# Performance work log

Measured on AMD Instinct MI355X. Metric: run time of the kernel, lower is better.

The kernel has to match this reference:

```python
import jax, jax.numpy as jnp
import numpy as np

N, D, R, E, B = 98304, 128, 3, 491520, 16384


def setup_inputs() -> dict:
    key = jax.random.key(0)
    ks = jax.random.split(key, 12)
    s = 0.05
    return {
        "latents": jax.random.normal(ks[0], (N, D), jnp.float32),
        "Wm": jax.random.normal(ks[1], (R, D, 2 * D), jnp.float32) * s,
        "bm": jax.random.normal(ks[2], (R, D), jnp.float32) * s,
        "W1": jax.random.normal(ks[3], (D, D), jnp.float32) * s,
        "b1": jax.random.normal(ks[4], (D,), jnp.float32) * s,
        "W2": jax.random.normal(ks[5], (D, D), jnp.float32) * s,
        "b2": jax.random.normal(ks[6], (D,), jnp.float32) * s,
        "message_from": jax.random.randint(ks[7], (E,), 0, N),
        "message_to": jax.random.randint(ks[8], (E,), 0, N),
        "view_id": jax.random.randint(ks[9], (N,), 0, B),
        "ch": 6,
        "batch_size": B,
    }


def reference(latents, Wm, bm, W1, b1, W2, b2, message_from, message_to, view_id, ch, batch_size):
    # Message passing rounds: gather -> concat -> Linear+ReLU (dropout=identity in eval) -> scale -> scatter-add
    scale = 1.0 / (ch - 1)
    for r in range(Wm.shape[0]):
        h = jnp.concatenate([latents[message_from], latents[message_to]], axis=-1)  # [E, 2D]
        msg = jax.nn.relu(h @ Wm[r].T + bm[r]) * scale  # [E, D]
        latents = latents.at[message_to].add(msg)
    # Readout: sum latents per sample (note: original's `/ ch` result is discarded, so no division)
    y = jax.ops.segment_sum(latents, view_id, num_segments=batch_size)  # [B, D]
    h = jax.nn.relu(y @ W1.T + b1)
    return h @ W2.T + b2
```

## Files before the change

kernel.cpp:

```cpp
#include <hip/hip_runtime.h>

static constexpr int N  = 98304;
static constexpr int D  = 128;
static constexpr int E  = 491520;
static constexpr int B  = 16384;

using f32x4 = __attribute__((ext_vector_type(4))) float;
using s16x8 = __attribute__((ext_vector_type(8))) short;

typedef __attribute__((address_space(3))) void lds_void;
typedef const __attribute__((address_space(1))) void gbl_void;

__device__ __forceinline__ ushort f2bf(float x) {
    unsigned u = __float_as_uint(x);
    return (ushort)((u + 0x7fffu + ((u >> 16) & 1u)) >> 16);
}
__device__ __forceinline__ float bflo(unsigned u) { return __uint_as_float(u << 16); }
__device__ __forceinline__ float bfhi(unsigned u) { return __uint_as_float(u & 0xffff0000u); }

__global__ void zero2_kernel(int* __restrict__ p) {
    int i = blockIdx.x * 256 + threadIdx.x;
    if (i < N + B) p[i] = 0;
}

__global__ void hist2_kernel(const int* __restrict__ eto, const int* __restrict__ view,
                             int* __restrict__ cnt, int* __restrict__ vcnt) {
    int gid = blockIdx.x * 256 + threadIdx.x;
    if (gid < E) atomicAdd(&cnt[eto[gid]], 1);
    else if (gid < E + N) atomicAdd(&vcnt[view[gid - E]], 1);
}

__global__ __launch_bounds__(256) void scan1_kernel(const int* __restrict__ cnt, int* __restrict__ excl,
                                                    const int* __restrict__ vcnt, int* __restrict__ vexcl,
                                                    int* __restrict__ bsum) {
    __shared__ int s[256];
    const int b = blockIdx.x, t = threadIdx.x;
    const int* src; int* dst; int base;
    bool pad = (b < 96);
    if (pad) { src = cnt;  dst = excl;  base = b * 1024 + t * 4; }
    else     { src = vcnt; dst = vexcl; base = (b - 96) * 1024 + t * 4; }
    int4 v = *reinterpret_cast<const int4*>(src + base);
    if (pad) { v.x = (v.x + 3) & ~3; v.y = (v.y + 3) & ~3; v.z = (v.z + 3) & ~3; v.w = (v.w + 3) & ~3; }
    int local = v.x + v.y + v.z + v.w;
    s[t] = local; __syncthreads();
    for (int off = 1; off < 256; off <<= 1) {
        int x = (t >= off) ? s[t - off] : 0;
        __syncthreads();
        s[t] += x;
        __syncthreads();
    }
    int excl_t = s[t] - local;
    if (t == 255) bsum[b] = s[t];
    int4 o;
    o.x = excl_t; o.y = o.x + v.x; o.z = o.y + v.y; o.w = o.z + v.z;
    *reinterpret_cast<int4*>(dst + base) = o;
}

__global__ __launch_bounds__(128) void scan2_kernel(int* __restrict__ bsum) {
    __shared__ int s[128];
    const int t = threadIdx.x;
    int val = (t < 112) ? bsum[t] : 0;
    s[t] = val;
    __syncthreads();
    #pragma unroll
    for (int off = 1; off < 128; off <<= 1) {
        int x = (t >= off) ? s[t - off] : 0;
        __syncthreads();
        s[t] += x;
        __syncthreads();
    }
    int incl = s[t];
    int seg0_total = s[95];
    int excl = incl - val;
    if (t < 96) bsum[t] = excl;
    else if (t < 112) bsum[t] = excl - seg0_total;
}

__global__ void scan3_kernel(int* __restrict__ excl, int* __restrict__ vexcl,
                             const int* __restrict__ bsum) {
    int b = blockIdx.x, t = threadIdx.x;
    if (b < 384) { int i = b * 256 + t; excl[i] += bsum[i >> 10]; }
    else         { int i = (b - 384) * 256 + t; vexcl[i] += bsum[96 + (i >> 10)]; }
}

__global__ void scatter2_kernel(const int* __restrict__ efrom, const int* __restrict__ eto,
                                const int* __restrict__ view,
                                int* __restrict__ ecur, int* __restrict__ vcur,
                                int* __restrict__ sfrom, int* __restrict__ perm) {
    int gid = blockIdx.x * 256 + threadIdx.x;
    if (gid < E) {
        int p = atomicAdd(&ecur[eto[gid]], 1);
        sfrom[p] = efrom[gid];
    } else if (gid < E + N) {
        int n = gid - E;
        int p = atomicAdd(&vcur[view[n]], 1);
        perm[p] = n;
    }
}

__global__ void fillpad_kernel(const int* __restrict__ cur, int* __restrict__ sfrom) {
    int v = blockIdx.x * 256 + threadIdx.x;
    if (v >= N) return;
    int c = cur[v], e = (c + 3) & ~3;
    for (; c < e; ++c) sfrom[c] = N;
}

__global__ void sentinel_kernel(ushort* __restrict__ Z) {
    Z[(size_t)N * 256 + threadIdx.x] = 0xFF80;
}

__global__ void convUV_kernel(const float* __restrict__ Wm, ushort* __restrict__ Wf) {
    int gid = blockIdx.x * 256 + threadIdx.x;
    if (gid >= 3 * 32768) return;
    int r = gid >> 15, rem = gid & 32767;
    int j = rem & 7, lane = (rem >> 3) & 63, grp = rem >> 9;
    int kt = grp >> 4, nt = grp & 15;
    int n = (nt & 7) * 16 + (lane & 15);
    int k = kt * 32 + (lane >> 4) * 8 + j;
    int col = ((nt >> 3) << 7) + k;
    Wf[gid] = f2bf(Wm[((size_t)r * 128 + n) * 256 + col]);
}

__global__ void convW12_kernel(const float* __restrict__ W1, const float* __restrict__ W2,
                               ushort* __restrict__ Wb12) {
    int gid = blockIdx.x * 256 + threadIdx.x;
    if (gid >= 2 * 16384) return;
    int w = gid >> 14, rem = gid & 16383;
    int n = rem >> 7, k = rem & 127;
    int kt = k >> 5, nt = n >> 4;
    int lane = (n & 15) + (((k >> 3) & 3) << 4);
    int j = k & 7;
    const float* W = w ? W2 : W1;
    Wb12[w * 16384 + ((kt * 8 + nt) * 64 + lane) * 8 + j] = f2bf(W[rem]);
}

__global__ __launch_bounds__(512) void uv_kernel(
    const float* __restrict__ Asrc, ushort* __restrict__ Z,
    const ushort* __restrict__ Wft, const float* __restrict__ bm_r)
{
    __shared__ alignas(16) ushort wlds[32768];
    const int t = threadIdx.x;

    #pragma unroll
    for (int it = 0; it < 8; ++it) {
        int idx = t + it * 512;
        __builtin_amdgcn_global_load_lds((gbl_void*)(Wft + idx * 8),
                                         (lds_void*)(wlds + idx * 8), 16, 0, 0);
    }

    const int wave = t >> 6, lane = t & 63;
    const int col16 = lane & 15, kq = lane >> 4;
    const int arow = blockIdx.x * 128 + wave * 16 + col16;

    const float4* Ar = reinterpret_cast<const float4*>(Asrc + (size_t)arow * 128);
    float4 areg[8];
    #pragma unroll
    for (int kt = 0; kt < 4; ++kt) {
        areg[2 * kt]     = Ar[kt * 8 + kq * 2];
        areg[2 * kt + 1] = Ar[kt * 8 + kq * 2 + 1];
    }

    f32x4 acc[16];
    #pragma unroll
    for (int nt = 0; nt < 16; ++nt) acc[nt] = (f32x4){0.f, 0.f, 0.f, 0.f};

    __syncthreads();

    const char* wb = reinterpret_cast<const char*>(wlds);
    #pragma unroll
    for (int kt = 0; kt < 4; ++kt) {
        float4 a0 = areg[2 * kt], a1 = areg[2 * kt + 1];
        union { s16x8 v; ushort u[8]; } pk;
        pk.u[0] = f2bf(a0.x); pk.u[1] = f2bf(a0.y); pk.u[2] = f2bf(a0.z); pk.u[3] = f2bf(a0.w);
        pk.u[4] = f2bf(a1.x); pk.u[5] = f2bf(a1.y); pk.u[6] = f2bf(a1.z); pk.u[7] = f2bf(a1.w);
        #pragma unroll
        for (int nt = 0; nt < 16; ++nt) {
            s16x8 wfr = *reinterpret_cast<const s16x8*>(wb + (((kt * 16 + nt) * 64 + lane) << 4));
            acc[nt] = __builtin_amdgcn_mfma_f32_16x16x32_bf16(wfr, pk.v, acc[nt], 0, 0, 0);
        }
    }

    ushort* zr = Z + (size_t)arow * 256;
    #pragma unroll
    for (int nt = 0; nt < 16; ++nt) {
        float4 bq;
        if (nt >= 8) bq = *reinterpret_cast<const float4*>(bm_r + (nt - 8) * 16 + kq * 4);
        else         bq = (float4){0.f, 0.f, 0.f, 0.f};
        union { uint2 d; ushort u[4]; } pk4;
        pk4.u[0] = f2bf(acc[nt][0] + bq.x);
        pk4.u[1] = f2bf(acc[nt][1] + bq.y);
        pk4.u[2] = f2bf(acc[nt][2] + bq.z);
        pk4.u[3] = f2bf(acc[nt][3] + bq.w);
        int cbase = ((nt >> 3) << 7) + (nt & 7) * 16 + kq * 4;
        *reinterpret_cast<uint2*>(zr + cbase) = pk4.d;
    }
}

__global__ __launch_bounds__(256) void edge_sum_kernel(
    const ushort* __restrict__ Z, const float* __restrict__ Lsrc, float* __restrict__ Ldst,
    const int* __restrict__ sfrom, const int* __restrict__ ends, const int* __restrict__ ch_ptr)
{
    const int t = threadIdx.x;
    const int wave = t >> 6, lane = t & 63;
    const float scale = 1.0f / (float)(ch_ptr[0] - 1);
    const int v0 = blockIdx.x * 16 + wave * 4;

    int bnd[5];
    bnd[0] = (v0 == 0) ? 0 : ((ends[v0 - 1] + 3) & ~3);
    #pragma unroll
    for (int i = 0; i < 4; ++i) bnd[i + 1] = (ends[v0 + i] + 3) & ~3;

    unsigned vv[4]; float2 lold[4];
    #pragma unroll
    for (int i = 0; i < 4; ++i) {
        vv[i] = *reinterpret_cast<const unsigned*>(Z + (size_t)(v0 + i) * 256 + 128 + lane * 2);
        lold[i] = *reinterpret_cast<const float2*>(Lsrc + (size_t)(v0 + i) * 128 + lane * 2);
    }

    int idx[4][4];
    #pragma unroll
    for (int i = 0; i < 4; ++i) {
        #pragma unroll
        for (int k = 0; k < 4; ++k) {
            int c = bnd[i] + k;
            idx[i][k] = (c < bnd[i + 1]) ? sfrom[c] : N;
        }
    }
    unsigned u[4][4];
    #pragma unroll
    for (int i = 0; i < 4; ++i)
        #pragma unroll
        for (int k = 0; k < 4; ++k)
            u[i][k] = *reinterpret_cast<const unsigned*>(Z + (size_t)idx[i][k] * 256 + lane * 2);

    #pragma unroll
    for (int i = 0; i < 4; ++i) {
        const float vl = bflo(vv[i]), vh = bfhi(vv[i]);
        float a0 = 0.f, a1 = 0.f;
        #pragma unroll
        for (int k = 0; k < 4; ++k) {
            a0 += fmaxf(bflo(u[i][k]) + vl, 0.f);
            a1 += fmaxf(bfhi(u[i][k]) + vh, 0.f);
        }
        for (int e = bnd[i] + 4; e < bnd[i + 1]; e += 4) {
            int f0 = sfrom[e], f1 = sfrom[e + 1], f2 = sfrom[e + 2], f3 = sfrom[e + 3];
            unsigned w0 = *reinterpret_cast<const unsigned*>(Z + (size_t)f0 * 256 + lane * 2);
            unsigned w1 = *reinterpret_cast<const unsigned*>(Z + (size_t)f1 * 256 + lane * 2);
            unsigned w2 = *reinterpret_cast<const unsigned*>(Z + (size_t)f2 * 256 + lane * 2);
            unsigned w3 = *reinterpret_cast<const unsigned*>(Z + (size_t)f3 * 256 + lane * 2);
            a0 += fmaxf(bflo(w0) + vl, 0.f) + fmaxf(bflo(w1) + vl, 0.f)
                + fmaxf(bflo(w2) + vl, 0.f) + fmaxf(bflo(w3) + vl, 0.f);
            a1 += fmaxf(bfhi(w0) + vh, 0.f) + fmaxf(bfhi(w1) + vh, 0.f)
                + fmaxf(bfhi(w2) + vh, 0.f) + fmaxf(bfhi(w3) + vh, 0.f);
        }
        float2 o;
        o.x = lold[i].x + scale * a0;
        o.y = lold[i].y + scale * a1;
        *reinterpret_cast<float2*>(Ldst + (size_t)(v0 + i) * 128 + lane * 2) = o;
    }
}

__global__ __launch_bounds__(256) void segsum_sorted_kernel(
    const float* __restrict__ L, const int* __restrict__ perm,
    const int* __restrict__ vends, float* __restrict__ y)
{
    const int t = threadIdx.x;
    const int wave = t >> 6, lane = t & 63;
    const int v = blockIdx.x * 4 + wave;
    const int lo = (v == 0) ? 0 : vends[v - 1];
    const int hi = vends[v];

    float a0 = 0.f, a1 = 0.f;
    for (int e = lo; e < hi; e += 2) {
        int last = hi - 1;
        int e1 = (e + 1 < hi) ? e + 1 : last;
        float m1 = (e + 1 < hi) ? 1.f : 0.f;
        int n0 = perm[e], n1 = perm[e1];
        float2 x0 = *reinterpret_cast<const float2*>(L + (size_t)n0 * 128 + lane * 2);
        float2 x1 = *reinterpret_cast<const float2*>(L + (size_t)n1 * 128 + lane * 2);
        a0 += x0.x + m1 * x1.x;
        a1 += x0.y + m1 * x1.y;
    }
    float2 o; o.x = a0; o.y = a1;
    *reinterpret_cast<float2*>(y + (size_t)v * 128 + lane * 2) = o;
}

__global__ __launch_bounds__(256) void readout_mfma_kernel(
    const float* __restrict__ y, float* __restrict__ outp,
    const ushort* __restrict__ Wb1, const ushort* __restrict__ Wb2,
    const float* __restrict__ b1, const float* __restrict__ b2)
{
    __shared__ alignas(16) ushort hs[64 * 128];
    const int t = threadIdx.x;
    const int r0 = blockIdx.x * 64;
    char* hbase = reinterpret_cast<char*>(hs);
    const float4* y4 = reinterpret_cast<const float4*>(y);

    #pragma unroll
    for (int it = 0; it < 4; ++it) {
        int c = t + it * 256;
        int e = c >> 4, p = c & 15;
        int g = p ^ (e & 15);
        float4 a = y4[(size_t)(r0 + e) * 32 + g * 2];
        float4 bq = y4[(size_t)(r0 + e) * 32 + g * 2 + 1];
        union { s16x8 v; ushort u[8]; } pk;
        pk.u[0] = f2bf(a.x); pk.u[1] = f2bf(a.y); pk.u[2] = f2bf(a.z); pk.u[3] = f2bf(a.w);
        pk.u[4] = f2bf(bq.x); pk.u[5] = f2bf(bq.y); pk.u[6] = f2bf(bq.z); pk.u[7] = f2bf(bq.w);
        *reinterpret_cast<s16x8*>(hbase + e * 256 + p * 16) = pk.v;
    }
    __syncthreads();

    const int wave = t >> 6, lane = t & 63;
    const int rrow = wave * 16 + (lane & 15);
    const int kq = lane >> 4;
    const int rx = rrow & 15;
    const char* hrow = hbase + rrow * 256;
    const int col16 = lane & 15;

    f32x4 acc[8];
    #pragma unroll
    for (int nt = 0; nt < 8; ++nt) acc[nt] = (f32x4){0.f, 0.f, 0.f, 0.f};
    const s16x8* wf1 = reinterpret_cast<const s16x8*>(Wb1);
    #pragma unroll
    for (int kt = 0; kt < 4; ++kt) {
        int C = kt * 4 + kq;
        s16x8 a = *reinterpret_cast<const s16x8*>(hrow + ((C ^ rx) & 15) * 16);
        #pragma unroll
        for (int nt = 0; nt < 8; ++nt)
            acc[nt] = __builtin_amdgcn_mfma_f32_16x16x32_bf16(a, wf1[(kt * 8 + nt) * 64 + lane], acc[nt], 0, 0, 0);
    }
    __syncthreads();

    #pragma unroll
    for (int nt = 0; nt < 8; ++nt) {
        float bias = b1[nt * 16 + col16];
        #pragma unroll
        for (int j = 0; j < 4; ++j) {
            int r = wave * 16 + (lane >> 4) * 4 + j;
            float h = fmaxf(acc[nt][j] + bias, 0.f);
            int colfull = nt * 16 + col16;
            int chunk = colfull >> 3;
            int bo = ((chunk ^ (r & 15)) * 16) + (colfull & 7) * 2;
            *reinterpret_cast<ushort*>(hbase + r * 256 + bo) = f2bf(h);
        }
    }
    __syncthreads();

    f32x4 acc2[8];
    #pragma unroll
    for (int nt = 0; nt < 8; ++nt) acc2[nt] = (f32x4){0.f, 0.f, 0.f, 0.f};
    const s16x8* wf2 = reinterpret_cast<const s16x8*>(Wb2);
    #pragma unroll
    for (int kt = 0; kt < 4; ++kt) {
        int C = kt * 4 + kq;
        s16x8 a = *reinterpret_cast<const s16x8*>(hrow + ((C ^ rx) & 15) * 16);
        #pragma unroll
        for (int nt = 0; nt < 8; ++nt)
            acc2[nt] = __builtin_amdgcn_mfma_f32_16x16x32_bf16(a, wf2[(kt * 8 + nt) * 64 + lane], acc2[nt], 0, 0, 0);
    }

    #pragma unroll
    for (int nt = 0; nt < 8; ++nt) {
        float bias = b2[nt * 16 + col16];
        #pragma unroll
        for (int j = 0; j < 4; ++j) {
            int r = r0 + wave * 16 + (lane >> 4) * 4 + j;
            outp[(size_t)r * 128 + nt * 16 + col16] = acc2[nt][j] + bias;
        }
    }
}

extern "C" void kernel_launch(void* const* d_in, const int* in_sizes, int n_in,
                              void* d_out, int out_size, void* d_ws, size_t ws_size,
                              hipStream_t stream) {
    const float* latents = (const float*)d_in[0];
    const float* Wm      = (const float*)d_in[1];
    const float* bm      = (const float*)d_in[2];
    const float* W1      = (const float*)d_in[3];
    const float* b1      = (const float*)d_in[4];
    const float* W2      = (const float*)d_in[5];
    const float* b2      = (const float*)d_in[6];
    const int*   efrom   = (const int*)d_in[7];
    const int*   eto     = (const int*)d_in[8];
    const int*   view    = (const int*)d_in[9];
    const int*   ch      = (const int*)d_in[10];

    float*  L  = (float*)d_ws;
    ushort* Z  = (ushort*)(L + (size_t)N * D);
    float*  yb = (float*)Z;
    ushort* Wb12 = (ushort*)((char*)Z + 8388608);

    char* ob = (char*)d_out;
    ushort* WUVf = (ushort*)ob;
    int* cnt   = (int*)(ob + 196608);
    int* vcnt  = cnt + N;
    int* excl  = vcnt + B;
    int* vexcl = excl + N;
    int* bsum  = vexcl + B;
    int* sfrom = bsum + 128;
    int* perm  = sfrom + E + 3 * N;
    float* outp = (float*)d_out;

    convUV_kernel<<<384, 256, 0, stream>>>(Wm, WUVf);
    zero2_kernel<<<(N + B) / 256, 256, 0, stream>>>(cnt);
    hist2_kernel<<<(E + N) / 256, 256, 0, stream>>>(eto, view, cnt, vcnt);
    scan1_kernel<<<112, 256, 0, stream>>>(cnt, excl, vcnt, vexcl, bsum);
    scan2_kernel<<<1, 128, 0, stream>>>(bsum);
    scan3_kernel<<<448, 256, 0, stream>>>(excl, vexcl, bsum);
    scatter2_kernel<<<(E + N) / 256, 256, 0, stream>>>(efrom, eto, view, excl, vexcl, sfrom, perm);
    fillpad_kernel<<<N / 256, 256, 0, stream>>>(excl, sfrom);
    sentinel_kernel<<<1, 256, 0, stream>>>(Z);

    uv_kernel<<<N / 128, 512, 0, stream>>>(latents, Z, WUVf, bm);
    edge_sum_kernel<<<N / 16, 256, 0, stream>>>(Z, latents, L, sfrom, excl, ch);
    uv_kernel<<<N / 128, 512, 0, stream>>>(L, Z, WUVf + 32768, bm + D);
    edge_sum_kernel<<<N / 16, 256, 0, stream>>>(Z, L, L, sfrom, excl, ch);
    uv_kernel<<<N / 128, 512, 0, stream>>>(L, Z, WUVf + 65536, bm + 2 * D);
    edge_sum_kernel<<<N / 16, 256, 0, stream>>>(Z, L, L, sfrom, excl, ch);

    convW12_kernel<<<128, 256, 0, stream>>>(W1, W2, Wb12);
    segsum_sorted_kernel<<<B / 4, 256, 0, stream>>>(L, perm, vexcl, yb);
    readout_mfma_kernel<<<B / 64, 256, 0, stream>>>(yb, outp, Wb12, Wb12 + 16384, b1, b2);
}
```

Measured before the change: 309.2 us.

## Merge setup kernels and prefetch edge indices as int4 in edge_sum

Drops the fillpad and sentinel kernels. The whole sfrom array is now pre-filled with the sentinel index inside a grid-stride zeroing kernel, and the sentinel row write is folded into the weight-conversion kernel. Empty nodes are padded to one group of 4 sentinel edges. This lets edge_sum load indices as aligned int4 with a one-step software prefetch instead of per-element guarded loads. It saves two launches and simplifies the gather loop, but writes extra sentinel entries, adds wasted sentinel gathers for empty nodes, and issues an extra int4 load past each segment.

```diff
diff --git a/kernel.cpp b/kernel.cpp
--- a/kernel.cpp
+++ b/kernel.cpp
@@ -4,6 +4,7 @@
 static constexpr int D  = 128;
 static constexpr int E  = 491520;
 static constexpr int B  = 16384;
+static constexpr int SFN = E + 4 * N + 64;
 
 using f32x4 = __attribute__((ext_vector_type(4))) float;
 using s16x8 = __attribute__((ext_vector_type(8))) short;
@@ -18,9 +19,11 @@
 __device__ __forceinline__ float bflo(unsigned u) { return __uint_as_float(u << 16); }
 __device__ __forceinline__ float bfhi(unsigned u) { return __uint_as_float(u & 0xffff0000u); }
 
-__global__ void zero2_kernel(int* __restrict__ p) {
-    int i = blockIdx.x * 256 + threadIdx.x;
-    if (i < N + B) p[i] = 0;
+__global__ void setup_fill_kernel(int* __restrict__ cnt, int* __restrict__ sfrom) {
+    int i = blockIdx.x * blockDim.x + threadIdx.x;
+    int stride = gridDim.x * blockDim.x;
+    for (int j = i; j < N + B; j += stride) cnt[j] = 0;
+    for (int j = i; j < SFN; j += stride) sfrom[j] = N;
 }
 
 __global__ void hist2_kernel(const int* __restrict__ eto, const int* __restrict__ view,
@@ -40,7 +43,12 @@
     if (pad) { src = cnt;  dst = excl;  base = b * 1024 + t * 4; }
     else     { src = vcnt; dst = vexcl; base = (b - 96) * 1024 + t * 4; }
     int4 v = *reinterpret_cast<const int4*>(src + base);
-    if (pad) { v.x = (v.x + 3) & ~3; v.y = (v.y + 3) & ~3; v.z = (v.z + 3) & ~3; v.w = (v.w + 3) & ~3; }
+    if (pad) {
+        v.x = (v.x == 0) ? 4 : ((v.x + 3) & ~3);
+        v.y = (v.y == 0) ? 4 : ((v.y + 3) & ~3);
+        v.z = (v.z == 0) ? 4 : ((v.z + 3) & ~3);
+        v.w = (v.w == 0) ? 4 : ((v.w + 3) & ~3);
+    }
     int local = v.x + v.y + v.z + v.w;
     s[t] = local; __syncthreads();
     for (int off = 1; off < 256; off <<= 1) {
@@ -98,27 +106,20 @@
     }
 }
 
-__global__ void fillpad_kernel(const int* __restrict__ cur, int* __restrict__ sfrom) {
-    int v = blockIdx.x * 256 + threadIdx.x;
-    if (v >= N) return;
-    int c = cur[v], e = (c + 3) & ~3;
-    for (; c < e; ++c) sfrom[c] = N;
-}
-
-__global__ void sentinel_kernel(ushort* __restrict__ Z) {
-    Z[(size_t)N * 256 + threadIdx.x] = 0xFF80;
-}
-
-__global__ void convUV_kernel(const float* __restrict__ Wm, ushort* __restrict__ Wf) {
+__global__ void convUV_kernel(const float* __restrict__ Wm, ushort* __restrict__ Wf,
+                              ushort* __restrict__ Z) {
     int gid = blockIdx.x * 256 + threadIdx.x;
-    if (gid >= 3 * 32768) return;
-    int r = gid >> 15, rem = gid & 32767;
-    int j = rem & 7, lane = (rem >> 3) & 63, grp = rem >> 9;
-    int kt = grp >> 4, nt = grp & 15;
-    int n = (nt & 7) * 16 + (lane & 15);
-    int k = kt * 32 + (lane >> 4) * 8 + j;
-    int col = ((nt >> 3) << 7) + k;
-    Wf[gid] = f2bf(Wm[((size_t)r * 128 + n) * 256 + col]);
+    if (gid < 3 * 32768) {
+        int r = gid >> 15, rem = gid & 32767;
+        int j = rem & 7, lane = (rem >> 3) & 63, grp = rem >> 9;
+        int kt = grp >> 4, nt = grp & 15;
+        int n = (nt & 7) * 16 + (lane & 15);
+        int k = kt * 32 + (lane >> 4) * 8 + j;
+        int col = ((nt >> 3) << 7) + k;
+        Wf[gid] = f2bf(Wm[((size_t)r * 128 + n) * 256 + col]);
+    } else if (gid < 3 * 32768 + 256) {
+        Z[(size_t)N * 256 + (gid - 3 * 32768)] = 0xFF80;
+    }
 }
 
 __global__ void convW12_kernel(const float* __restrict__ W1, const float* __restrict__ W2,
@@ -217,41 +218,23 @@
         lold[i] = *reinterpret_cast<const float2*>(Lsrc + (size_t)(v0 + i) * 128 + lane * 2);
     }
 
-    int idx[4][4];
-    #pragma unroll
-    for (int i = 0; i < 4; ++i) {
-        #pragma unroll
-        for (int k = 0; k < 4; ++k) {
-            int c = bnd[i] + k;
-            idx[i][k] = (c < bnd[i + 1]) ? sfrom[c] : N;
-        }
-    }
-    unsigned u[4][4];
-    #pragma unroll
-    for (int i = 0; i < 4; ++i)
-        #pragma unroll
-        for (int k = 0; k < 4; ++k)
-            u[i][k] = *reinterpret_cast<const unsigned*>(Z + (size_t)idx[i][k] * 256 + lane * 2);
+    int4 cur = *reinterpret_cast<const int4*>(sfrom + bnd[0]);
 
     #pragma unroll
     for (int i = 0; i < 4; ++i) {
         const float vl = bflo(vv[i]), vh = bfhi(vv[i]);
         float a0 = 0.f, a1 = 0.f;
-        #pragma unroll
-        for (int k = 0; k < 4; ++k) {
-            a0 += fmaxf(bflo(u[i][k]) + vl, 0.f);
-            a1 += fmaxf(bfhi(u[i][k]) + vh, 0.f);
-        }
-        for (int e = bnd[i] + 4; e < bnd[i + 1]; e += 4) {
-            int f0 = sfrom[e], f1 = sfrom[e + 1], f2 = sfrom[e + 2], f3 = sfrom[e + 3];
-            unsigned w0 = *reinterpret_cast<const unsigned*>(Z + (size_t)f0 * 256 + lane * 2);
-            unsigned w1 = *reinterpret_cast<const unsigned*>(Z + (size_t)f1 * 256 + lane * 2);
-            unsigned w2 = *reinterpret_cast<const unsigned*>(Z + (size_t)f2 * 256 + lane * 2);
-            unsigned w3 = *reinterpret_cast<const unsigned*>(Z + (size_t)f3 * 256 + lane * 2);
+        for (int e = bnd[i]; e < bnd[i + 1]; e += 4) {
+            int4 nxt = *reinterpret_cast<const int4*>(sfrom + e + 4);
+            unsigned w0 = *reinterpret_cast<const unsigned*>(Z + (size_t)cur.x * 256 + lane * 2);
+            unsigned w1 = *reinterpret_cast<const unsigned*>(Z + (size_t)cur.y * 256 + lane * 2);
+            unsigned w2 = *reinterpret_cast<const unsigned*>(Z + (size_t)cur.z * 256 + lane * 2);
+            unsigned w3 = *reinterpret_cast<const unsigned*>(Z + (size_t)cur.w * 256 + lane * 2);
             a0 += fmaxf(bflo(w0) + vl, 0.f) + fmaxf(bflo(w1) + vl, 0.f)
                 + fmaxf(bflo(w2) + vl, 0.f) + fmaxf(bflo(w3) + vl, 0.f);
             a1 += fmaxf(bfhi(w0) + vh, 0.f) + fmaxf(bfhi(w1) + vh, 0.f)
                 + fmaxf(bfhi(w2) + vh, 0.f) + fmaxf(bfhi(w3) + vh, 0.f);
+            cur = nxt;
         }
         float2 o;
         o.x = lold[i].x + scale * a0;
@@ -398,18 +381,16 @@
     int* vexcl = excl + N;
     int* bsum  = vexcl + B;
     int* sfrom = bsum + 128;
-    int* perm  = sfrom + E + 3 * N;
+    int* perm  = sfrom + SFN;
     float* outp = (float*)d_out;
 
-    convUV_kernel<<<384, 256, 0, stream>>>(Wm, WUVf);
-    zero2_kernel<<<(N + B) / 256, 256, 0, stream>>>(cnt);
+    convUV_kernel<<<385, 256, 0, stream>>>(Wm, WUVf, Z);
+    setup_fill_kernel<<<2048, 256, 0, stream>>>(cnt, sfrom);
     hist2_kernel<<<(E + N) / 256, 256, 0, stream>>>(eto, view, cnt, vcnt);
     scan1_kernel<<<112, 256, 0, stream>>>(cnt, excl, vcnt, vexcl, bsum);
     scan2_kernel<<<1, 128, 0, stream>>>(bsum);
     scan3_kernel<<<448, 256, 0, stream>>>(excl, vexcl, bsum);
     scatter2_kernel<<<(E + N) / 256, 256, 0, stream>>>(efrom, eto, view, excl, vexcl, sfrom, perm);
-    fillpad_kernel<<<N / 256, 256, 0, stream>>>(excl, sfrom);
-    sentinel_kernel<<<1, 256, 0, stream>>>(Z);
 
     uv_kernel<<<N / 128, 512, 0, stream>>>(latents, Z, WUVf, bm);
     edge_sum_kernel<<<N / 16, 256, 0, stream>>>(Z, latents, L, sfrom, excl, ch);
```

Result: faster. 286.8 us (-7.2%).
